# Kernel tuning notes

Measured on AMD Instinct MI355X. Metric: run time of the kernel, lower is better.

## Reference

```python
import jax, jax.numpy as jnp
import numpy as np
import math

H = 8
D_MODEL = 512
D_K = D_MODEL // H          # 64, per-head value dim
D_QK = D_K // 2             # 32, per-head query/key dim
B, S = 2, 4096


def setup_inputs() -> dict:
    key = jax.random.key(0)
    ks = jax.random.split(key, 20)
    std = 0.02
    inp = {
        'query': jax.random.normal(ks[0], (B, S, D_MODEL), jnp.float32),
        'key':   jax.random.normal(ks[1], (B, S, D_MODEL), jnp.float32),
        'value': jax.random.normal(ks[2], (B, S, D_MODEL), jnp.float32),
        # MLP_q: d_model -> 2*d_model -> d_model/2
        'Wq1': jax.random.normal(ks[3], (D_MODEL, 2 * D_MODEL), jnp.float32) * std,
        'bq1': jnp.zeros((2 * D_MODEL,), jnp.float32),
        'Wq2': jax.random.normal(ks[4], (2 * D_MODEL, D_MODEL // 2), jnp.float32) * std,
        'bq2': jnp.zeros((D_MODEL // 2,), jnp.float32),
        # MLP_k: d_model -> 2*d_model -> d_model/2
        'Wk1': jax.random.normal(ks[5], (D_MODEL, 2 * D_MODEL), jnp.float32) * std,
        'bk1': jnp.zeros((2 * D_MODEL,), jnp.float32),
        'Wk2': jax.random.normal(ks[6], (2 * D_MODEL, D_MODEL // 2), jnp.float32) * std,
        'bk2': jnp.zeros((D_MODEL // 2,), jnp.float32),
        # linear_v and output linear: d_model -> d_model
        'Wv': jax.random.normal(ks[7], (D_MODEL, D_MODEL), jnp.float32) * std,
        'bv': jnp.zeros((D_MODEL,), jnp.float32),
        'Wo': jax.random.normal(ks[8], (D_MODEL, D_MODEL), jnp.float32) * std,
        'bo': jnp.zeros((D_MODEL,), jnp.float32),
    }
    return inp


def reference(query, key, value, Wq1, bq1, Wq2, bq2, Wk1, bk1, Wk2, bk2, Wv, bv, Wo, bo):
    nb = query.shape[0]
    # MLP_q / MLP_k: Linear -> exact GELU -> Linear (torch GELU default is erf)
    q = jax.nn.gelu(query @ Wq1 + bq1, approximate=False) @ Wq2 + bq2   # [B,S,D_MODEL/2]
    k = jax.nn.gelu(key   @ Wk1 + bk1, approximate=False) @ Wk2 + bk2   # [B,S,D_MODEL/2]
    v = value @ Wv + bv                                                  # [B,S,D_MODEL]

    q = q.reshape(nb, -1, H, D_QK)   # [B,S,H,d_qk]
    k = k.reshape(nb, -1, H, D_QK)
    v = v.reshape(nb, -1, H, D_K)    # [B,S,H,d_k]

    # scores scaled by sqrt(d_qk) since query.size(-1) == d_k//2 in the original
    scores = jnp.einsum('bqhd,bkhd->bhqk', q, k) / math.sqrt(D_QK)  # [B,H,S,S]
    p = jax.nn.softmax(scores, axis=-1)
    x = jnp.einsum('bhqk,bkhd->bqhd', p, v).reshape(nb, -1, H * D_K)  # [B,S,D_MODEL]
    return x @ Wo + bo
```

## Files before the change

### kernel.cpp

```cpp
#include <hip/hip_runtime.h>
#include <math.h>

typedef __attribute__((ext_vector_type(8))) short short8;
typedef __bf16 bf16x8 __attribute__((ext_vector_type(8)));
typedef __attribute__((ext_vector_type(4))) float f32x4;
typedef __attribute__((ext_vector_type(2))) float f32x2;
typedef __attribute__((ext_vector_type(16))) float f32x16;
typedef __attribute__((ext_vector_type(4))) unsigned uint4v;

__device__ inline short f2bf(float f) {
    unsigned u = __builtin_bit_cast(unsigned, f);
    u += 0x7fff + ((u >> 16) & 1);
    return (short)(u >> 16);
}
__device__ inline float gelu_f(float x) {
    return 0.5f * x * (1.f + erff(x * 0.70710678118654752f));
}

__device__ inline void gload_lds16(const void* g, void* l) {
    __builtin_amdgcn_global_load_lds(
        (const __attribute__((address_space(1))) unsigned int*)g,
        (__attribute__((address_space(3))) unsigned int*)l, 16, 0, 0);
}

__global__ __launch_bounds__(256) void prep_w(
    const float* __restrict__ Wq1, const float* __restrict__ Wk1,
    const float* __restrict__ Wq2, const float* __restrict__ Wk2,
    const float* __restrict__ Wv,  const float* __restrict__ Wo,
    short* __restrict__ Wq1t, short* __restrict__ Wk1t,
    short* __restrict__ Wq2t, short* __restrict__ Wk2t,
    short* __restrict__ Wvt,  short* __restrict__ Wot)
{
    int id = blockIdx.x;
    const float* W; short* Wt; int K, N;
    if (id < 512)       { W = Wq1; Wt = Wq1t; K = 512;  N = 1024; }
    else if (id < 1024) { W = Wk1; Wt = Wk1t; K = 512;  N = 1024; id -= 512; }
    else if (id < 1280) { W = Wq2; Wt = Wq2t; K = 1024; N = 256;  id -= 1024; }
    else if (id < 1536) { W = Wk2; Wt = Wk2t; K = 1024; N = 256;  id -= 1280; }
    else if (id < 1792) { W = Wv;  Wt = Wvt;  K = 512;  N = 512;  id -= 1536; }
    else                { W = Wo;  Wt = Wot;  K = 512;  N = 512;  id -= 1792; }
    int nx = N >> 5;
    int n0 = (id % nx) * 32, k0 = (id / nx) * 32;

    __shared__ float T[32][33];
    int tid = threadIdx.x;
    int r = tid >> 3, c4 = (tid & 7) * 4;
    float4 v4 = *(const float4*)&W[(size_t)(k0 + r) * N + n0 + c4];
    T[r][c4 + 0] = v4.x; T[r][c4 + 1] = v4.y; T[r][c4 + 2] = v4.z; T[r][c4 + 3] = v4.w;
    __syncthreads();
    short4 o;
    o.x = f2bf(T[c4 + 0][r]);
    o.y = f2bf(T[c4 + 1][r]);
    o.z = f2bf(T[c4 + 2][r]);
    o.w = f2bf(T[c4 + 3][r]);
    *(short4*)&Wt[(size_t)(n0 + r) * K + k0 + c4] = o;
}

template <int BM, int BN, int AF32>
__device__ __forceinline__ void gemm_core(
    const void* __restrict__ A, const short* __restrict__ B,
    const float* __restrict__ bias, void* __restrict__ C_,
    float scale, int act, int om, int nbn, int N, int K, int L)
{
    constexpr int MT = BM / 32;
    constexpr int NT = BN / 32;
    const int xcd = L & 7;
    const int per = L >> 3;
    const int bn = (per % nbn) * BN;
    const int bm = ((per / nbn) * 8 + xcd) * BM;

    const int tid = threadIdx.x;
    const int w = tid >> 6;
    const int lane = tid & 63;
    const int l15 = lane & 15, quad = lane >> 4;
    const int wm = (w >> 1) * (BM / 2), wn = (w & 1) * (BN / 2);

    __shared__ __align__(16) short As[BM * 64];
    __shared__ __align__(16) short Bs[BN * 64];

    f32x4 acc[MT][NT];
#pragma unroll
    for (int mt = 0; mt < MT; ++mt)
#pragma unroll
        for (int nt = 0; nt < NT; ++nt) acc[mt][nt] = (f32x4){0.f, 0.f, 0.f, 0.f};

    for (int k0 = 0; k0 < K; k0 += 64) {
#pragma unroll
        for (int i = 0; i < BM / 32; ++i) {
            int ga = tid + i * 256;
            int row = ga >> 3, g = ga & 7;
            if constexpr (AF32) {
                const float* Af = (const float*)A;
                const float* src = &Af[(size_t)(bm + row) * K + k0 + ((g ^ (row & 7)) * 8)];
                float4 x = *(const float4*)src;
                float4 y = *(const float4*)(src + 4);
                unsigned u0, u1, u2, u3;
                asm("v_cvt_pk_bf16_f32 %0, %1, %2" : "=v"(u0) : "v"(x.x), "v"(x.y));
                asm("v_cvt_pk_bf16_f32 %0, %1, %2" : "=v"(u1) : "v"(x.z), "v"(x.w));
                asm("v_cvt_pk_bf16_f32 %0, %1, %2" : "=v"(u2) : "v"(y.x), "v"(y.y));
                asm("v_cvt_pk_bf16_f32 %0, %1, %2" : "=v"(u3) : "v"(y.z), "v"(y.w));
                uint4v u; u[0] = u0; u[1] = u1; u[2] = u2; u[3] = u3;
                *(uint4v*)(void*)&As[row * 64 + g * 8] = u;
            } else {
                const short* Ab = (const short*)A;
                gload_lds16(&Ab[(size_t)(bm + row) * K + k0 + ((g ^ (row & 7)) * 8)],
                            &As[(i * 256 + w * 64) * 8]);
            }
        }
#pragma unroll
        for (int i = 0; i < BN / 32; ++i) {
            int gb = tid + i * 256;
            int row = gb >> 3, g = gb & 7;
            gload_lds16(&B[(size_t)(bn + row) * K + k0 + ((g ^ (row & 7)) * 8)],
                        &Bs[(i * 256 + w * 64) * 8]);
        }
        __syncthreads();

#pragma unroll
        for (int ks = 0; ks < 2; ++ks) {
            bf16x8 af[MT], bfr[NT];
#pragma unroll
            for (int t = 0; t < MT; ++t) {
                int row = wm + t * 16 + l15;
                af[t] = __builtin_bit_cast(bf16x8,
                    *(const short8*)(const void*)&As[row * 64 + (((ks * 4 + quad) ^ (row & 7)) * 8)]);
            }
#pragma unroll
            for (int t = 0; t < NT; ++t) {
                int row = wn + t * 16 + l15;
                bfr[t] = __builtin_bit_cast(bf16x8,
                    *(const short8*)(const void*)&Bs[row * 64 + (((ks * 4 + quad) ^ (row & 7)) * 8)]);
            }
#pragma unroll
            for (int mt = 0; mt < MT; ++mt)
#pragma unroll
                for (int nt = 0; nt < NT; ++nt)
                    acc[mt][nt] = __builtin_amdgcn_mfma_f32_16x16x32_bf16(af[mt], bfr[nt], acc[mt][nt], 0, 0, 0);
        }
        __syncthreads();
    }

    float bvv[NT];
#pragma unroll
    for (int nt = 0; nt < NT; ++nt) bvv[nt] = bias[bn + wn + nt * 16 + l15];
#pragma unroll
    for (int mt = 0; mt < MT; ++mt)
#pragma unroll
        for (int r = 0; r < 4; ++r) {
            int row = bm + wm + mt * 16 + quad * 4 + r;
#pragma unroll
            for (int nt = 0; nt < NT; ++nt) {
                float v = acc[mt][nt][r] + bvv[nt];
                if (act) v = gelu_f(v);
                v *= scale;
                int col = bn + wn + nt * 16 + l15;
                if (om == 1) {
                    ((float*)C_)[(size_t)row * N + col] = v;
                } else if (om == 2) {
                    int b_ = row >> 12, key = row & 4095;
                    int kt = key >> 6, nt_ = (key >> 5) & 1, l31_ = key & 31;
                    int h_ = col >> 5, kcol = col & 31;
                    int ks_ = kcol >> 4, hi_ = (kcol >> 3) & 1, j_ = kcol & 7;
                    size_t idx = ((((size_t)(b_ * 8 + h_) * 64 + kt) * 4 +
                                   (nt_ * 2 + ks_)) * 64 + (hi_ * 32 + l31_)) * 8 + j_;
                    ((short*)C_)[idx] = f2bf(v);
                } else if (om == 3) {
                    int b_ = row >> 12, key = row & 4095;
                    int kt = key >> 6, keyr = key & 63;
                    int ks_ = keyr >> 4, hi_ = (keyr >> 3) & 1, j_ = keyr & 7;
                    int h_ = col >> 6, dk = col & 63;
                    int dt_ = dk >> 5, l31_ = dk & 31;
                    size_t idx = ((((size_t)(b_ * 8 + h_) * 64 + kt) * 8 +
                                   (dt_ * 4 + ks_)) * 64 + (hi_ * 32 + l31_)) * 8 + j_;
                    ((short*)C_)[idx] = f2bf(v);
                } else {
                    ((short*)C_)[(size_t)row * N + col] = f2bf(v);
                }
            }
        }
}

__global__ __launch_bounds__(256) void mega1(
    const float* __restrict__ q, const float* __restrict__ k,
    const float* __restrict__ v,
    const short* __restrict__ Wq1t, const short* __restrict__ Wk1t,
    const short* __restrict__ Wvt,
    const float* __restrict__ bq1, const float* __restrict__ bk1,
    const float* __restrict__ bv,
    short* __restrict__ H1q, short* __restrict__ H1k, short* __restrict__ vfr)
{
    const int z = blockIdx.z;
    if (z == 2 && blockIdx.x >= 256) return;
    const float* A   = z == 2 ? v    : (z == 1 ? k    : q);
    const short* B   = z == 2 ? Wvt  : (z == 1 ? Wk1t : Wq1t);
    const float* bia = z == 2 ? bv   : (z == 1 ? bk1  : bq1);
    void*        C   = z == 2 ? (void*)vfr : (z == 1 ? (void*)H1k : (void*)H1q);
    const int act = z == 2 ? 0 : 1;
    const int om  = z == 2 ? 3 : 0;
    const int nbn = z == 2 ? 4 : 8;
    const int N   = z == 2 ? 512 : 1024;
    gemm_core<128, 128, 1>(A, B, bia, C, 1.f, act, om, nbn, N, 512, blockIdx.x);
}

__global__ __launch_bounds__(256) void gemm2k(
    const short* __restrict__ H1q, const short* __restrict__ H1k,
    const short* __restrict__ Wq2t, const short* __restrict__ Wk2t,
    const float* __restrict__ bq2, const float* __restrict__ bk2,
    short* __restrict__ qbb, short* __restrict__ kfr, float qscale)
{
    const int z = blockIdx.z;
    const short* A   = z ? H1k : H1q;
    const short* B   = z ? Wk2t : Wq2t;
    const float* bia = z ? bk2 : bq2;
    void*        C   = z ? (void*)kfr : (void*)qbb;
    const float  sc  = z ? 1.f : qscale;
    const int    om  = z ? 2 : 0;
    gemm_core<64, 64, 0>(A, B, bia, C, sc, 0, om, 4, 256, 1024, blockIdx.x);
}

__global__ __launch_bounds__(256) void gemmok(
    const short* __restrict__ xbb, const short* __restrict__ Wot,
    const float* __restrict__ bo, float* __restrict__ out)
{
    gemm_core<64, 64, 0>(xbb, Wot, bo, out, 1.f, 0, 1, 8, 512, 512, blockIdx.x);
}

__global__ __launch_bounds__(256, 4) void flash_ks(
    const short* __restrict__ qb, const short* __restrict__ kfr,
    const short* __restrict__ vfr, short* __restrict__ xbb)
{
    const int L = blockIdx.x;
    const int xcd = L & 7;
    const int idx = L >> 3;
    const int bh = xcd * 2 + (idx & 1);
    const int qt = idx >> 1;
    const int b = bh >> 3, h = bh & 7;
    const int w = threadIdx.x >> 6;
    const int qg = w >> 1;
    const int kh = w & 1;
    const int lane = threadIdx.x & 63;
    const int l31 = lane & 31;
    const int half = lane >> 5;

    __shared__ __align__(16) char smem[17408];

    const short* qrow = qb + (size_t)(b * 4096 + qt * 64 + qg * 32 + l31) * 256 + h * 32 + half * 8;
    bf16x8 qf0 = __builtin_bit_cast(bf16x8, *(const short8*)(const void*)qrow);
    bf16x8 qf1 = __builtin_bit_cast(bf16x8, *(const short8*)(const void*)(qrow + 16));

    f32x16 O0{}, O1{};
    f32x2 lp = (f32x2){0.f, 0.f};

    const short* kbase = kfr + ((size_t)bh * 64) * 4 * 512 + lane * 8;
    const short* vbase = vfr + ((size_t)bh * 64) * 8 * 512 + lane * 8;

#pragma unroll 1
    for (int t = 0; t < 32; ++t) {
        const int kt = kh * 32 + t;
        bf16x8 kc[4], vc[8];
        const short* kp = kbase + (size_t)kt * 4 * 512;
        const short* vp = vbase + (size_t)kt * 8 * 512;
#pragma unroll
        for (int c = 0; c < 4; ++c)
            kc[c] = __builtin_bit_cast(bf16x8, *(const short8*)(const void*)(kp + c * 512));
#pragma unroll
        for (int c = 0; c < 8; ++c)
            vc[c] = __builtin_bit_cast(bf16x8, *(const short8*)(const void*)(vp + c * 512));

        f32x16 zero{};
        f32x16 s0 = __builtin_amdgcn_mfma_f32_32x32x16_bf16(kc[0], qf0, zero, 0, 0, 0);
        s0 = __builtin_amdgcn_mfma_f32_32x32x16_bf16(kc[1], qf1, s0, 0, 0, 0);
        f32x16 s1 = __builtin_amdgcn_mfma_f32_32x32x16_bf16(kc[2], qf0, zero, 0, 0, 0);
        s1 = __builtin_amdgcn_mfma_f32_32x32x16_bf16(kc[3], qf1, s1, 0, 0, 0);

        bf16x8 pf[4];
#pragma unroll
        for (int nt = 0; nt < 2; ++nt) {
            const f32x16& s = nt ? s1 : s0;
            float p0  = __builtin_amdgcn_exp2f(s[0]);
            float p1  = __builtin_amdgcn_exp2f(s[1]);
            float p2  = __builtin_amdgcn_exp2f(s[2]);
            float p3  = __builtin_amdgcn_exp2f(s[3]);
            float p4  = __builtin_amdgcn_exp2f(s[4]);
            float p5  = __builtin_amdgcn_exp2f(s[5]);
            float p6  = __builtin_amdgcn_exp2f(s[6]);
            float p7  = __builtin_amdgcn_exp2f(s[7]);
            float p8  = __builtin_amdgcn_exp2f(s[8]);
            float p9  = __builtin_amdgcn_exp2f(s[9]);
            float p10 = __builtin_amdgcn_exp2f(s[10]);
            float p11 = __builtin_amdgcn_exp2f(s[11]);
            float p12 = __builtin_amdgcn_exp2f(s[12]);
            float p13 = __builtin_amdgcn_exp2f(s[13]);
            float p14 = __builtin_amdgcn_exp2f(s[14]);
            float p15 = __builtin_amdgcn_exp2f(s[15]);

            lp += (f32x2){p0,  p1};
            lp += (f32x2){p2,  p3};
            lp += (f32x2){p4,  p5};
            lp += (f32x2){p6,  p7};
            lp += (f32x2){p8,  p9};
            lp += (f32x2){p10, p11};
            lp += (f32x2){p12, p13};
            lp += (f32x2){p14, p15};

            unsigned D0, D1, D2, D3, D4, D5, D6, D7;
            asm("v_cvt_pk_bf16_f32 %0, %1, %2" : "=v"(D0) : "v"(p0),  "v"(p1));
            asm("v_cvt_pk_bf16_f32 %0, %1, %2" : "=v"(D1) : "v"(p2),  "v"(p3));
            asm("v_cvt_pk_bf16_f32 %0, %1, %2" : "=v"(D2) : "v"(p4),  "v"(p5));
            asm("v_cvt_pk_bf16_f32 %0, %1, %2" : "=v"(D3) : "v"(p6),  "v"(p7));
            asm("v_cvt_pk_bf16_f32 %0, %1, %2" : "=v"(D4) : "v"(p8),  "v"(p9));
            asm("v_cvt_pk_bf16_f32 %0, %1, %2" : "=v"(D5) : "v"(p10), "v"(p11));
            asm("v_cvt_pk_bf16_f32 %0, %1, %2" : "=v"(D6) : "v"(p12), "v"(p13));
            asm("v_cvt_pk_bf16_f32 %0, %1, %2" : "=v"(D7) : "v"(p14), "v"(p15));
            asm("v_permlane32_swap_b32 %0, %1" : "+v"(D0), "+v"(D2));
            asm("v_permlane32_swap_b32 %0, %1" : "+v"(D1), "+v"(D3));
            asm("v_permlane32_swap_b32 %0, %1" : "+v"(D4), "+v"(D6));
            asm("v_permlane32_swap_b32 %0, %1" : "+v"(D5), "+v"(D7));
            uint4v u0; u0[0] = D0; u0[1] = D1; u0[2] = D2; u0[3] = D3;
            uint4v u1; u1[0] = D4; u1[1] = D5; u1[2] = D6; u1[3] = D7;
            pf[2 * nt + 0] = __builtin_bit_cast(bf16x8, u0);
            pf[2 * nt + 1] = __builtin_bit_cast(bf16x8, u1);
        }

#pragma unroll
        for (int ks = 0; ks < 4; ++ks) {
            O0 = __builtin_amdgcn_mfma_f32_32x32x16_bf16(pf[ks], vc[ks], O0, 0, 0, 0);
            O1 = __builtin_amdgcn_mfma_f32_32x32x16_bf16(pf[ks], vc[4 + ks], O1, 0, 0, 0);
        }
    }

    float lsum = lp[0] + lp[1];
    float lother = lsum;
    asm("v_permlane32_swap_b32 %0, %1" : "+v"(lsum), "+v"(lother));
    lsum += lother;

    float* redO = (float*)smem;
    float* redl = (float*)(smem + 16896);
    if (half == 0)
        redl[(qg * 2 + kh) * 32 + l31] = lsum;
    if (kh == 1) {
        float* Bo = redO + qg * 32 * 66;
#pragma unroll
        for (int r = 0; r < 16; ++r) {
            int q = (r & 3) + 8 * (r >> 2) + 4 * half;
            Bo[q * 66 + l31] = O0[r];
            Bo[q * 66 + 32 + l31] = O1[r];
        }
    }
    __syncthreads();
    if (kh == 0) {
        const float* Bo = redO + qg * 32 * 66;
#pragma unroll
        for (int r = 0; r < 16; ++r) {
            int q = (r & 3) + 8 * (r >> 2) + 4 * half;
            float o0 = O0[r] + Bo[q * 66 + l31];
            float o1 = O1[r] + Bo[q * 66 + 32 + l31];
            float inv = 1.f / (redl[(qg * 2 + 0) * 32 + q] + redl[(qg * 2 + 1) * 32 + q]);
            size_t row = (size_t)(b * 4096 + qt * 64 + qg * 32 + q);
            short* d = xbb + row * 512 + h * 64 + l31;
            d[0] = f2bf(o0 * inv);
            d[32] = f2bf(o1 * inv);
        }
    }
}

extern "C" void kernel_launch(void* const* d_in, const int* in_sizes, int n_in,
                              void* d_out, int out_size, void* d_ws, size_t ws_size,
                              hipStream_t stream)
{
    const float* query = (const float*)d_in[0];
    const float* key   = (const float*)d_in[1];
    const float* value = (const float*)d_in[2];
    const float* Wq1   = (const float*)d_in[3];
    const float* bq1   = (const float*)d_in[4];
    const float* Wq2   = (const float*)d_in[5];
    const float* bq2   = (const float*)d_in[6];
    const float* Wk1   = (const float*)d_in[7];
    const float* bk1   = (const float*)d_in[8];
    const float* Wk2   = (const float*)d_in[9];
    const float* bk2   = (const float*)d_in[10];
    const float* Wv    = (const float*)d_in[11];
    const float* bv    = (const float*)d_in[12];
    const float* Wo    = (const float*)d_in[13];
    const float* bo    = (const float*)d_in[14];
    float* out = (float*)d_out;

    char* ws = (char*)d_ws;
    short* H1q   = (short*)(ws + 0);
    short* H1k   = (short*)(ws + 16777216);
    short* xbb   = (short*)(ws + 0);
    short* qbb   = (short*)(ws + 33554432);
    short* kfr   = (short*)(ws + 50331648);
    short* vfr   = (short*)(ws + 54525952);
    short* Wq1t  = (short*)(ws + 62914560);
    short* Wk1t  = (short*)(ws + 63963136);
    short* Wq2t  = (short*)(ws + 65011712);
    short* Wk2t  = (short*)(ws + 65536000);
    short* Wvt   = (short*)(ws + 66060288);
    short* Wot   = (short*)(ws + 66584576);

    dim3 blk(256);
    const float qscale = 0.17677669529663687f * 1.4426950408889634f;

    prep_w<<<dim3(2048), blk, 0, stream>>>(
        Wq1, Wk1, Wq2, Wk2, Wv, Wo, Wq1t, Wk1t, Wq2t, Wk2t, Wvt, Wot);

    mega1<<<dim3(512, 1, 3), blk, 0, stream>>>(
        query, key, value, Wq1t, Wk1t, Wvt, bq1, bk1, bv, H1q, H1k, vfr);

    gemm2k<<<dim3(512, 1, 2), blk, 0, stream>>>(
        H1q, H1k, Wq2t, Wk2t, bq2, bk2, qbb, kfr, qscale);

    flash_ks<<<dim3(1024), blk, 0, stream>>>(qbb, kfr, vfr, xbb);

    gemmok<<<dim3(1024), blk, 0, stream>>>(xbb, Wot, bo, out);
}
```

Before: 268.1 us.

## Double-buffer GEMM LDS tiles to overlap global loads with MFMA compute

Converts the projection GEMM core's main loop into a two-stage software pipeline with double-buffered LDS tiles. The next K-tile's global loads are issued, into registers for the fp32 A path or straight to LDS for bf16, before computing on the current tile, and the loads are completed and converted after the MFMAs. This aims to hide global memory latency behind compute and cut one barrier per iteration. It doubles LDS usage and adds registers for the staged fp32 A data, which may lower occupancy.

```diff
diff --git a/kernel.cpp b/kernel.cpp
--- a/kernel.cpp
+++ b/kernel.cpp
@@ -75,36 +75,26 @@
     const int l15 = lane & 15, quad = lane >> 4;
     const int wm = (w >> 1) * (BM / 2), wn = (w & 1) * (BN / 2);
 
-    __shared__ __align__(16) short As[BM * 64];
-    __shared__ __align__(16) short Bs[BN * 64];
-
-    f32x4 acc[MT][NT];
-#pragma unroll
-    for (int mt = 0; mt < MT; ++mt)
-#pragma unroll
-        for (int nt = 0; nt < NT; ++nt) acc[mt][nt] = (f32x4){0.f, 0.f, 0.f, 0.f};
-
-    for (int k0 = 0; k0 < K; k0 += 64) {
+    __shared__ __align__(16) short As[2][BM * 64];
+    __shared__ __align__(16) short Bs[2][BN * 64];
+
+    const float* Af = (const float*)A;
+    const short* Ab = (const short*)A;
+
+    float4 xa[BM / 32], ya[BM / 32];
+
+    auto stage_issue = [&](int k0, int buf) {
 #pragma unroll
         for (int i = 0; i < BM / 32; ++i) {
             int ga = tid + i * 256;
             int row = ga >> 3, g = ga & 7;
             if constexpr (AF32) {
-                const float* Af = (const float*)A;
                 const float* src = &Af[(size_t)(bm + row) * K + k0 + ((g ^ (row & 7)) * 8)];
-                float4 x = *(const float4*)src;
-                float4 y = *(const float4*)(src + 4);
-                unsigned u0, u1, u2, u3;
-                asm("v_cvt_pk_bf16_f32 %0, %1, %2" : "=v"(u0) : "v"(x.x), "v"(x.y));
-                asm("v_cvt_pk_bf16_f32 %0, %1, %2" : "=v"(u1) : "v"(x.z), "v"(x.w));
-                asm("v_cvt_pk_bf16_f32 %0, %1, %2" : "=v"(u2) : "v"(y.x), "v"(y.y));
-                asm("v_cvt_pk_bf16_f32 %0, %1, %2" : "=v"(u3) : "v"(y.z), "v"(y.w));
-                uint4v u; u[0] = u0; u[1] = u1; u[2] = u2; u[3] = u3;
-                *(uint4v*)(void*)&As[row * 64 + g * 8] = u;
+                xa[i] = *(const float4*)src;
+                ya[i] = *(const float4*)(src + 4);
             } else {
-                const short* Ab = (const short*)A;
                 gload_lds16(&Ab[(size_t)(bm + row) * K + k0 + ((g ^ (row & 7)) * 8)],
-                            &As[(i * 256 + w * 64) * 8]);
+                            &As[buf][(i * 256 + w * 64) * 8]);
             }
         }
 #pragma unroll
@@ -112,24 +102,60 @@
             int gb = tid + i * 256;
             int row = gb >> 3, g = gb & 7;
             gload_lds16(&B[(size_t)(bn + row) * K + k0 + ((g ^ (row & 7)) * 8)],
-                        &Bs[(i * 256 + w * 64) * 8]);
-        }
-        __syncthreads();
-
+                        &Bs[buf][(i * 256 + w * 64) * 8]);
+        }
+    };
+    auto stage_finish = [&](int buf) {
+        asm volatile("s_waitcnt vmcnt(0)");
+        if constexpr (AF32) {
+#pragma unroll
+            for (int i = 0; i < BM / 32; ++i) {
+                int ga = tid + i * 256;
+                int row = ga >> 3, g = ga & 7;
+                unsigned u0, u1, u2, u3;
+                asm("v_cvt_pk_bf16_f32 %0, %1, %2" : "=v"(u0) : "v"(xa[i].x), "v"(xa[i].y));
+                asm("v_cvt_pk_bf16_f32 %0, %1, %2" : "=v"(u1) : "v"(xa[i].z), "v"(xa[i].w));
+                asm("v_cvt_pk_bf16_f32 %0, %1, %2" : "=v"(u2) : "v"(ya[i].x), "v"(ya[i].y));
+                asm("v_cvt_pk_bf16_f32 %0, %1, %2" : "=v"(u3) : "v"(ya[i].z), "v"(ya[i].w));
+                uint4v u; u[0] = u0; u[1] = u1; u[2] = u2; u[3] = u3;
+                *(uint4v*)(void*)&As[buf][row * 64 + g * 8] = u;
+            }
+        }
+    };
+
+    f32x4 acc[MT][NT];
+#pragma unroll
+    for (int mt = 0; mt < MT; ++mt)
+#pragma unroll
+        for (int nt = 0; nt < NT; ++nt) acc[mt][nt] = (f32x4){0.f, 0.f, 0.f, 0.f};
+
+    const int ntile = K >> 6;
+
+    stage_issue(0, 0);
+    stage_finish(0);
+    __syncthreads();
+
+    int cur = 0;
+    for (int t = 0; t < ntile; ++t) {
+        const bool has_next = (t + 1 < ntile);
+        if (has_next) stage_issue((t + 1) << 6, cur ^ 1);
+
+        const short* Asc = As[cur];
+        const short* Bsc = Bs[cur];
 #pragma unroll
         for (int ks = 0; ks < 2; ++ks) {
             bf16x8 af[MT], bfr[NT];
 #pragma unroll
-            for (int t = 0; t < MT; ++t) {
-                int row = wm + t * 16 + l15;
-                af[t] = __builtin_bit_cast(bf16x8,
-                    *(const short8*)(const void*)&As[row * 64 + (((ks * 4 + quad) ^ (row & 7)) * 8)]);
+            for (int t2 = 0; t2 < MT; ++t2) {
+                int row = wm + t2 * 16 + l15;
+                af[t2] = __builtin_bit_cast(bf16x8,
+                    *(const short8*)(const void*)&Asc[row * 64 + (((ks * 4 + quad) ^ (row & 7)) * 8)]);
             }
 #pragma unroll
-            for (int t = 0; t < NT; ++t) {
-                int row = wn + t * 16 + l15;
-                bfr[t] = __builtin_bit_cast(bf16x8,
-                    *(const short8*)(const void*)&Bs[row * 64 + (((ks * 4 + quad) ^ (row & 7)) * 8)]);
+            for (int t2 = 0; t2 < NT; ++t2) {
+                int row = wn + t2 * 16 + l15;
+                bfr[t2] = __builtin_bit_cast(bf16x8,
+                    *(const short8*)(const void*)&Bsc[row * 64 + (((ks * 4 + quad) ^ (row & 7)) * 8)]);
             }
 #pragma unroll
             for (int mt = 0; mt < MT; ++mt)
@@ -137,7 +163,10 @@
                 for (int nt = 0; nt < NT; ++nt)
                     acc[mt][nt] = __builtin_amdgcn_mfma_f32_16x16x32_bf16(af[mt], bfr[nt], acc[mt][nt], 0, 0, 0);
         }
+
+        if (has_next) stage_finish(cur ^ 1);
         __syncthreads();
+        cur ^= 1;
     }
 
     float bvv[NT];
```

New measurement: 302.1 us. 1.13x slower.
